# Optimization experiments

Hardware: AMD Instinct MI355X
Metric: run time of the kernel (lower is better)

## Reference

```python
import jax, jax.numpy as jnp
import numpy as np

N_NODES = 100000
N_EDGES = 500000
D = 128        # node feat dim == output dim
DT = 128       # time encoding dim
DE = 128       # edge feat dim
B = 300
K = 2
NN = 20
N_HEADS = 2
N_LAYERS = 2


def setup_inputs() -> dict:
    key = jax.random.key(0)
    ks = jax.random.split(key, 20)
    s = 0.05
    inp = {
        "node_features": jax.random.normal(ks[0], (N_NODES, D), jnp.float32) * s,
        "edge_features": jax.random.normal(ks[1], (N_EDGES, DE), jnp.float32) * s,
        "time_w": jax.random.normal(ks[2], (1, DT), jnp.float32),
        "time_b": jax.random.normal(ks[3], (DT,), jnp.float32),
        "Wq": jax.random.normal(ks[4], (N_LAYERS, D + DT, D), jnp.float32) * s,
        "Wk": jax.random.normal(ks[5], (N_LAYERS, D + DT + DE, D), jnp.float32) * s,
        "Wv": jax.random.normal(ks[6], (N_LAYERS, D + DT + DE, D), jnp.float32) * s,
        "Wo": jax.random.normal(ks[7], (N_LAYERS, D, D), jnp.float32) * s,
        "fc1": jax.random.normal(ks[8], (N_LAYERS, 2 * D, D), jnp.float32) * s,
        "fc2": jax.random.normal(ks[9], (N_LAYERS, D, D), jnp.float32) * s,
        "source_nodes": jax.random.randint(ks[10], (B,), 0, N_NODES),
        "timestamps": jax.random.uniform(ks[11], (B,), jnp.float32, 500.0, 1000.0),
        "neigh2": jax.random.randint(ks[12], (B, K, NN), 0, N_NODES),
        "eidx2": jax.random.randint(ks[13], (B, K, NN), 0, N_EDGES),
        "etimes2": jax.random.uniform(ks[14], (B, K, NN), jnp.float32, 0.0, 500.0),
        "neigh1": jax.random.randint(ks[15], (B * K * NN, K, NN), 0, N_NODES),
        "eidx1": jax.random.randint(ks[16], (B * K * NN, K, NN), 0, N_EDGES),
        "etimes1": jax.random.uniform(ks[17], (B * K * NN, K, NN), jnp.float32, 0.0, 500.0),
    }
    return inp


def reference(node_features, edge_features, time_w, time_b,
              Wq, Wk, Wv, Wo, fc1, fc2,
              source_nodes, timestamps,
              neigh2, eidx2, etimes2,
              neigh1, eidx1, etimes1):
    d = node_features.shape[1]
    dh = d // N_HEADS

    def time_enc(t):  # t: [...] -> [..., DT], TGAT-style cosine time encoding
        return jnp.cos(t[..., None] * time_w[0] + time_b)

    def hop_agg(layer, src_nodes, ts, neigh, eidx, etimes, neigh_emb):
        # neigh/eidx/etimes: [b, K, NN]; neigh_emb: [b, K, NN, d]
        b = src_nodes.shape[0]
        kn = K * NN
        src = node_features[src_nodes]                         # [b, d]
        src_t = time_enc(jnp.zeros((b,), ts.dtype))            # [b, DT]
        deltas = ts[:, None, None] - etimes                    # [b, K, NN]
        et = time_enc(deltas.reshape(b, kn))                   # [b, kn, DT]
        ef = edge_features[eidx].reshape(b, kn, -1)            # [b, kn, DE]
        ne = neigh_emb.reshape(b, kn, -1)                      # [b, kn, d]
        mask = neigh.reshape(b, kn) == 0                       # padded neighbors

        q = jnp.concatenate([src, src_t], axis=-1) @ Wq[layer]            # [b, d]
        kv_in = jnp.concatenate([ne, et, ef], axis=-1)                    # [b, kn, d+DT+DE]
        kk = kv_in @ Wk[layer]                                            # [b, kn, d]
        vv = kv_in @ Wv[layer]

        qh = q.reshape(b, N_HEADS, dh)
        kh = kk.reshape(b, kn, N_HEADS, dh)
        vh = vv.reshape(b, kn, N_HEADS, dh)
        scores = jnp.einsum('bhd,bnhd->bhn', qh, kh) / jnp.sqrt(jnp.float32(dh))
        scores = jnp.where(mask[:, None, :], jnp.float32(-1e9), scores)
        attn = jax.nn.softmax(scores, axis=-1)                            # [b, h, kn]
        out = jnp.einsum('bhn,bnhd->bhd', attn, vh).reshape(b, d) @ Wo[layer]
        merged = jnp.concatenate([out, src], axis=-1)                     # [b, 2d]
        return jax.nn.relu(merged @ fc1[layer]) @ fc2[layer]              # [b, d]

    # --- recursion unrolled (n_layers = 2) ---
    # level 0: raw node features of 2-hop neighbors
    b1 = neigh2.shape[0] * K * NN
    emb0 = node_features[neigh1.reshape(-1)].reshape(b1, K, NN, d)
    ts1 = jnp.repeat(timestamps, K * NN)
    # level 1 aggregation (attention_models[0])
    emb1 = hop_agg(0, neigh2.reshape(-1), ts1, neigh1, eidx1, etimes1, emb0)
    # level 2 aggregation (attention_models[1])
    emb2 = hop_agg(1, source_nodes, timestamps,
                   neigh2, eidx2, etimes2,
                   emb1.reshape(source_nodes.shape[0], K, NN, d))
    return emb2
```

## Files before the change

### kernel.cpp

```cpp
#include <hip/hip_runtime.h>
#include <cstdint>

typedef _Float16 half_t;
typedef _Float16 half8  __attribute__((ext_vector_type(8)));
typedef _Float16 half4_t __attribute__((ext_vector_type(4)));
typedef _Float16 h2f    __attribute__((ext_vector_type(2)));
typedef float    floatx4 __attribute__((ext_vector_type(4)));

#define KNN 40
#define KVPAD 124

#define WS_NF16    0ull
#define WS_EMB16   25600000ull
#define WS_WKVT    28672000ull
#define WS_WQ4     29065216ull
#define WS_W1A4    29196288ull
#define WS_W1B4    29327360ull
#define WS_W24     29458432ull
#define WS_QBIAS   29589504ull
#define WS_WOFTMP  29590528ull
#define WS_ZERO    29721600ull
#define WS_EF16    29721856ull
#define WS_TOTAL_FULL (WS_EF16 + 128000000ull)

__device__ __forceinline__ void ld16(const void* g, void* l) {
  __builtin_amdgcn_global_load_lds(
      (const __attribute__((address_space(1))) unsigned int*)(uintptr_t)g,
      (__attribute__((address_space(3))) unsigned int*)(uintptr_t)l, 16, 0, 0);
}

__device__ __forceinline__ float dot4(half4_t a, half4_t b, float s) {
  s = __builtin_amdgcn_fdot2((h2f){a[0], a[1]}, (h2f){b[0], b[1]}, s, false);
  s = __builtin_amdgcn_fdot2((h2f){a[2], a[3]}, (h2f){b[2], b[3]}, s, false);
  return s;
}

__global__ __launch_bounds__(256) void cvt_kernel(
    const float* __restrict__ src, half_t* __restrict__ dst, int n8) {
  int stride = gridDim.x * 256;
  for (int i = blockIdx.x * 256 + threadIdx.x; i < n8; i += stride) {
    float4 a = *((const float4*)src + 2 * (size_t)i);
    float4 b = *((const float4*)src + 2 * (size_t)i + 1);
    half8 h;
    h[0] = (half_t)a.x; h[1] = (half_t)a.y; h[2] = (half_t)a.z; h[3] = (half_t)a.w;
    h[4] = (half_t)b.x; h[5] = (half_t)b.y; h[6] = (half_t)b.z; h[7] = (half_t)b.w;
    *((half8*)dst + i) = h;
  }
}

#define PK_DECODE(t) int l = (t) >> 14; int u = (t) & 16383; \
  int d4 = u >> 9; int v = u & 511; int j = v >> 2; int e = v & 3;

__global__ __launch_bounds__(256) void precompute_w(
    const float* __restrict__ Wq, const float* __restrict__ Wk,
    const float* __restrict__ Wv, const float* __restrict__ Wo,
    const float* __restrict__ fc1, const float* __restrict__ fc2,
    const float* __restrict__ time_b,
    half_t* __restrict__ WkvT, float* __restrict__ qbias,
    float* __restrict__ woftmp, half_t* __restrict__ Wq4,
    half_t* __restrict__ W1b4, half_t* __restrict__ W24,
    half_t* __restrict__ zrow)
{
  int blk = blockIdx.x, tid = threadIdx.x;
  if (blk < 768) {
    int t = blk * 256 + tid;
    int l = t / 98304;
    int r = t - l * 98304;
    int n = r / 384;
    int k = r - n * 384;
    float vv = (n < 128) ? Wk[l * 49152 + k * 128 + n]
                         : Wv[l * 49152 + k * 128 + (n - 128)];
    WkvT[t] = (half_t)vv;
  } else if (blk == 768) {
    if (tid < 128) zrow[tid] = (half_t)0.f;
    int l = tid >> 7, j = tid & 127;
    float s = 0.f;
    for (int d = 0; d < 128; ++d)
      s += cosf(time_b[d]) * Wq[l * 32768 + (128 + d) * 128 + j];
    qbias[l * 128 + j] = s;
  } else if (blk < 897) {
    int t = (blk - 769) * 256 + tid;
    int l = t >> 14;
    int r = t & 16383;
    int dd = r >> 7, j = r & 127;
    float s = 0.f;
    for (int m = 0; m < 128; ++m)
      s += Wo[l * 16384 + dd * 128 + m] * fc1[l * 32768 + m * 128 + j];
    woftmp[t] = s;
  } else if (blk < 1025) {
    int t = (blk - 897) * 256 + tid;
    PK_DECODE(t);
    Wq4[t] = (half_t)Wq[l * 32768 + (4 * d4 + e) * 128 + j];
  } else if (blk < 1153) {
    int t = (blk - 1025) * 256 + tid;
    PK_DECODE(t);
    W1b4[t] = (half_t)fc1[l * 32768 + (128 + 4 * d4 + e) * 128 + j];
  } else {
    int t = (blk - 1153) * 256 + tid;
    PK_DECODE(t);
    W24[t] = (half_t)fc2[l * 16384 + (4 * d4 + e) * 128 + j];
  }
}

__global__ __launch_bounds__(256) void precompute_w2(
    const float* __restrict__ woftmp, half_t* __restrict__ W1a4) {
  int t = blockIdx.x * 256 + threadIdx.x;
  PK_DECODE(t);
  W1a4[t] = (half_t)woftmp[l * 16384 + (4 * d4 + e) * 128 + j];
}

template <bool EF16, bool L1DIR>
__global__ __launch_bounds__(512, 4) void hop_kernel(
    const float*  __restrict__ nf,
    const half_t* __restrict__ ne16,
    const half_t* __restrict__ ef16,
    const float*  __restrict__ ef32,
    const int*    __restrict__ src_idx,
    const float*  __restrict__ tsv,
    const int*    __restrict__ neigh,
    const int*    __restrict__ eidx,
    const float*  __restrict__ etimes,
    const float*  __restrict__ tw,
    const float*  __restrict__ tb,
    const half_t* __restrict__ Wq4_l,
    const float*  __restrict__ qbias_l,
    const half_t* __restrict__ WkvT_l,
    const half_t* __restrict__ W1a4_l,
    const half_t* __restrict__ W1b4_l,
    const half_t* __restrict__ W24_l,
    const half_t* __restrict__ zrow,
    half_t* __restrict__ out16,
    float*  __restrict__ out32)
{
  __shared__ __align__(16) char smem[71360];
  half_t* BTs  = (half_t*)(smem + 32768);
  half_t* kvT  = (half_t*)(smem + 32768);
  float*  tw_s = (float*)(smem + 65536);
  float*  tb_s = (float*)(smem + 66048);
  float*  qs   = (float*)(smem + 66560);
  half_t* s16  = (half_t*)(smem + 68096);
  half_t* aO16 = (half_t*)(smem + 68864);
  half_t* h116 = (half_t*)(smem + 69632);
  float*  scs  = (float*)(smem + 70400);

  const int tid = threadIdx.x;
  const int bbase = blockIdx.x * 3;
  const int lane = tid & 63, wv = tid >> 6;
  const int l15 = lane & 15, q4 = lane >> 4;
  const int wm = (wv & 1) * 64, wn = (wv >> 1) * 64;

  if (tid < 128) { tw_s[tid] = tw[tid]; tb_s[tid] = tb[tid]; }
  if (tid < 96) {
    int g = tid >> 5, d4 = tid & 31;
    float4 v4 = *(const float4*)(nf + (size_t)src_idx[bbase + g] * 128 + d4 * 4);
    half4_t h;
    h[0] = (half_t)v4.x; h[1] = (half_t)v4.y; h[2] = (half_t)v4.z; h[3] = (half_t)v4.w;
    *(half4_t*)(s16 + g * 128 + d4 * 4) = h;
  }

  const int r = wv * 16 + l15;
  const bool valid = (r < 120);
  float dval = 0.f;
  const half_t* pNE = zrow + q4 * 8;
  const half_t* pEF = zrow + q4 * 8;
  if (valid) {
    int g = r / 40, n = r - g * 40;
    int bg = bbase + g;
    int rowidx = bg * KNN + n;
    dval = tsv[L1DIR ? bg : (bg / 40)] - etimes[rowidx];
    pNE = (L1DIR ? ne16 + (size_t)rowidx * 128
                 : ne16 + (size_t)neigh[rowidx] * 128) + q4 * 8;
    if (EF16) pEF = ef16 + (size_t)eidx[rowidx] * 128 + q4 * 8;
  }
  const float* gbe32 = nullptr;
  const int rr = tid >> 2, pp = tid & 3;
  if (!EF16 && rr < 120) {
    int g2 = rr / 40, n2 = rr - g2 * 40;
    gbe32 = ef32 + (size_t)eidx[(bbase + g2) * KNN + n2] * 128 + pp * 16;
  }

  const half_t* bBase = WkvT_l + (size_t)(2 * wv * 16 + l15) * 384 + q4 * 8;

  floatx4 acc[4][4];
  #pragma unroll
  for (int mi = 0; mi < 4; ++mi)
    #pragma unroll
    for (int ni = 0; ni < 4; ++ni) acc[mi][ni] = (floatx4){0.f, 0.f, 0.f, 0.f};

  auto issueA = [&](const half_t* p, int koff, char* buf) {
    ld16(p + koff,      buf + wv * 2048);
    ld16(p + koff + 32, buf + wv * 2048 + 1024);
  };
  auto issueB = [&](int kc) {
    const half_t* bp = bBase + kc * 64;
    ld16(bp,          (char*)BTs + wv * 4096);
    ld16(bp + 32,     (char*)BTs + wv * 4096 + 1024);
    ld16(bp + 6144,   (char*)BTs + wv * 4096 + 2048);
    ld16(bp + 6176,   (char*)BTs + wv * 4096 + 3072);
  };
  auto cosA = [&](int koff, char* buf) {
    #pragma unroll
    for (int i = 0; i < 2; ++i) {
      int c = i * 4 + q4;
      half8 h;
      #pragma unroll
      for (int j = 0; j < 8; ++j) {
        float ang = __builtin_fmaf(dval, tw_s[koff + c * 8 + j], tb_s[koff + c * 8 + j]);
        h[j] = valid ? (half_t)__cosf(ang) : (half_t)0.f;
      }
      *(half8*)(buf + wv * 2048 + i * 1024 + lane * 16) = h;
    }
  };
  auto efA32 = [&](int koff, char* buf) {
    half8 h0 = {}, h1 = {};
    if (rr < 120) {
      const float* gb = gbe32 + koff;
      float4 v0 = ((const float4*)gb)[0];
      float4 v1 = ((const float4*)gb)[1];
      float4 v2 = ((const float4*)gb)[2];
      float4 v3 = ((const float4*)gb)[3];
      h0[0] = (half_t)v0.x; h0[1] = (half_t)v0.y; h0[2] = (half_t)v0.z; h0[3] = (half_t)v0.w;
      h0[4] = (half_t)v1.x; h0[5] = (half_t)v1.y; h0[6] = (half_t)v1.z; h0[7] = (half_t)v1.w;
      h1[0] = (half_t)v2.x; h1[1] = (half_t)v2.y; h1[2] = (half_t)v2.z; h1[3] = (half_t)v2.w;
      h1[4] = (half_t)v3.x; h1[5] = (half_t)v3.y; h1[6] = (half_t)v3.z; h1[7] = (half_t)v3.w;
    }
    half_t* Ad = (half_t*)buf + (((rr >> 4) * 8) + 2 * pp) * 128 + (rr & 15) * 8;
    *(half8*)Ad = h0;
    *(half8*)(Ad + 128) = h1;
  };
  auto mfma_step = [&](const char* abuf) {
    #pragma unroll
    for (int ks = 0; ks < 2; ++ks) {
      int c = ks * 4 + q4;
      half8 a[4];
      #pragma unroll
      for (int mi = 0; mi < 4; ++mi)
        a[mi] = *(const half8*)((const half_t*)abuf + (((wm >> 4) + mi) * 8 + c) * 128 + l15 * 8);
      #pragma unroll
      for (int ni = 0; ni < 4; ++ni) {
        half8 bfr = *(const half8*)(BTs + (((wn >> 4) + ni) * 8 + c) * 128 + l15 * 8);
        #pragma unroll
        for (int mi = 0; mi < 4; ++mi)
          acc[mi][ni] = __builtin_amdgcn_mfma_f32_16x16x32_f16(a[mi], bfr, acc[mi][ni], 0, 0, 0);
      }
    }
  };

  issueA(pNE, 0, smem);
  issueA(pNE, 64, smem + 16384);
  {
    const char* sw = (const char*)Wq4_l + wv * 4096 + lane * 16;
    char* dw = (char*)BTs + wv * 4096;
    ld16(sw, dw); ld16(sw + 1024, dw + 1024);
    ld16(sw + 2048, dw + 2048); ld16(sw + 3072, dw + 3072);
  }
  __syncthreads();

  if (tid < 384) {
    int gq = tid >> 7, jj = tid & 127;
    float s = qbias_l[jj];
    #pragma unroll 8
    for (int d4 = 0; d4 < 32; ++d4) {
      half4_t w = *(const half4_t*)(BTs + (d4 * 128 + jj) * 4);
      half4_t a = *(const half4_t*)(s16 + gq * 128 + d4 * 4);
      s = dot4(w, a, s);
    }
    qs[gq * 128 + jj] = s;
  }
  __syncthreads();

  issueB(0); __syncthreads(); mfma_step(smem);          __syncthreads();
  cosA(0, smem);
  issueB(1); __syncthreads(); mfma_step(smem + 16384);  __syncthreads();
  cosA(64, smem + 16384);
  issueB(2); __syncthreads(); mfma_step(smem);          __syncthreads();
  if (EF16) issueA(pEF, 0, smem); else efA32(0, smem);
  issueB(3); __syncthreads(); mfma_step(smem + 16384);  __syncthreads();
  if (EF16) issueA(pEF, 64, smem + 16384); else efA32(64, smem + 16384);
  issueB(4); __syncthreads(); mfma_step(smem);          __syncthreads();
  issueB(5); __syncthreads(); mfma_step(smem + 16384);  __syncthreads();

  {
    const char* sw = (const char*)W1a4_l + wv * 4096 + lane * 16;
    char* dw = smem + wv * 4096;
    ld16(sw, dw); ld16(sw + 1024, dw + 1024);
    ld16(sw + 2048, dw + 2048); ld16(sw + 3072, dw + 3072);
  }

  if (wv < 4) {
    #pragma unroll
    for (int mi = 0; mi < 4; ++mi) {
      int row0 = wm + mi * 16 + q4 * 4;
      if (row0 < 120) {
        #pragma unroll
        for (int ni = 0; ni < 4; ++ni) {
          int col = wn + ni * 16 + l15;
          half4_t h;
          h[0] = (half_t)acc[mi][ni][0]; h[1] = (half_t)acc[mi][ni][1];
          h[2] = (half_t)acc[mi][ni][2]; h[3] = (half_t)acc[mi][ni][3];
          *(half4_t*)(kvT + col * KVPAD + row0) = h;
        }
      }
    }
  }
  __syncthreads();

  if (tid < 240) {
    int g = tid / 80;
    int rem = tid - g * 80;
    int h = rem / 40;
    int n = rem - h * 40;
    bool masked = (neigh[(bbase + g) * KNN + n] == 0);
    const float* qrow = qs + g * 128 + h * 64;
    int row = g * 40 + n;
    float s = 0.f;
    #pragma unroll 8
    for (int d = 0; d < 64; ++d)
      s += qrow[d] * (float)kvT[(h * 64 + d) * KVPAD + row];
    scs[tid] = masked ? -1e9f : s * 0.125f;
  }
  __syncthreads();

  if (wv < 6) {
    float v = (lane < 40) ? scs[wv * 40 + lane] : -1e30f;
    float m = v;
    #pragma unroll
    for (int o = 32; o; o >>= 1) m = fmaxf(m, __shfl_xor(m, o));
    float e = (lane < 40) ? __expf(v - m) : 0.f;
    float ssum = e;
    #pragma unroll
    for (int o = 32; o; o >>= 1) ssum += __shfl_xor(ssum, o);
    if (lane < 40) scs[wv * 40 + lane] = e / ssum;
  }
  if (wv >= 4) {
    #pragma unroll
    for (int mi = 0; mi < 4; ++mi) {
      int row0 = wm + mi * 16 + q4 * 4;
      if (row0 < 120) {
        #pragma unroll
        for (int ni = 0; ni < 4; ++ni) {
          int col = wn - 128 + ni * 16 + l15;
          half4_t h;
          h[0] = (half_t)acc[mi][ni][0]; h[1] = (half_t)acc[mi][ni][1];
          h[2] = (half_t)acc[mi][ni][2]; h[3] = (half_t)acc[mi][ni][3];
          *(half4_t*)(kvT + col * KVPAD + row0) = h;
        }
      }
    }
  }
  __syncthreads();

  if (tid < 384) {
    int g = tid >> 7, dcol = tid & 127, h = dcol >> 6;
    const float* attn = scs + (g * 2 + h) * 40;
    const half_t* vcol = kvT + dcol * KVPAD + g * 40;
    float s = 0.f;
    #pragma unroll 8
    for (int n = 0; n < 40; ++n) s += attn[n] * (float)vcol[n];
    aO16[g * 128 + dcol] = (half_t)s;
  }
  __syncthreads();

  {
    const char* sw = (const char*)W1b4_l + wv * 4096 + lane * 16;
    char* dw = (char*)BTs + wv * 4096;
    ld16(sw, dw); ld16(sw + 1024, dw + 1024);
    ld16(sw + 2048, dw + 2048); ld16(sw + 3072, dw + 3072);
  }
  float p1 = 0.f;
  if (tid < 384) {
    int g = tid >> 7, jj = tid & 127;
    #pragma unroll 8
    for (int d4 = 0; d4 < 32; ++d4) {
      half4_t w = *(const half4_t*)((const half_t*)smem + (d4 * 128 + jj) * 4);
      half4_t a = *(const half4_t*)(aO16 + g * 128 + d4 * 4);
      p1 = dot4(w, a, p1);
    }
  }
  __syncthreads();

  {
    const char* sw = (const char*)W24_l + wv * 4096 + lane * 16;
    char* dw = smem + wv * 4096;
    ld16(sw, dw); ld16(sw + 1024, dw + 1024);
    ld16(sw + 2048, dw + 2048); ld16(sw + 3072, dw + 3072);
  }
  if (tid < 384) {
    int g = tid >> 7, jj = tid & 127;
    float p2 = p1;
    #pragma unroll 8
    for (int d4 = 0; d4 < 32; ++d4) {
      half4_t w = *(const half4_t*)(BTs + (d4 * 128 + jj) * 4);
      half4_t a = *(const half4_t*)(s16 + g * 128 + d4 * 4);
      p2 = dot4(w, a, p2);
    }
    h116[g * 128 + jj] = (half_t)fmaxf(p2, 0.f);
  }
  __syncthreads();

  if (tid < 384) {
    int g = tid >> 7, ii = tid & 127;
    float s = 0.f;
    #pragma unroll 8
    for (int j4 = 0; j4 < 32; ++j4) {
      half4_t w = *(const half4_t*)((const half_t*)smem + (j4 * 128 + ii) * 4);
      half4_t a = *(const half4_t*)(h116 + g * 128 + j4 * 4);
      s = dot4(w, a, s);
    }
    if (L1DIR) out32[(size_t)(bbase + g) * 128 + ii] = s;
    else       out16[(size_t)(bbase + g) * 128 + ii] = (half_t)s;
  }
}

extern "C" void kernel_launch(void* const* d_in, const int* in_sizes, int n_in,
                              void* d_out, int out_size, void* d_ws, size_t ws_size,
                              hipStream_t stream) {
  const float* nf      = (const float*)d_in[0];
  const float* ef      = (const float*)d_in[1];
  const float* tw      = (const float*)d_in[2];
  const float* tb      = (const float*)d_in[3];
  const float* Wq      = (const float*)d_in[4];
  const float* Wk      = (const float*)d_in[5];
  const float* Wv      = (const float*)d_in[6];
  const float* Wo      = (const float*)d_in[7];
  const float* fc1     = (const float*)d_in[8];
  const float* fc2     = (const float*)d_in[9];
  const int*   srcn    = (const int*)d_in[10];
  const float* ts      = (const float*)d_in[11];
  const int*   neigh2  = (const int*)d_in[12];
  const int*   eidx2   = (const int*)d_in[13];
  const float* etimes2 = (const float*)d_in[14];
  const int*   neigh1  = (const int*)d_in[15];
  const int*   eidx1   = (const int*)d_in[16];
  const float* etimes1 = (const float*)d_in[17];

  char* ws = (char*)d_ws;
  half_t* nf16   = (half_t*)(ws + WS_NF16);
  half_t* emb116 = (half_t*)(ws + WS_EMB16);
  half_t* WkvT16 = (half_t*)(ws + WS_WKVT);
  half_t* Wq4    = (half_t*)(ws + WS_WQ4);
  half_t* W1a4   = (half_t*)(ws + WS_W1A4);
  half_t* W1b4   = (half_t*)(ws + WS_W1B4);
  half_t* W24    = (half_t*)(ws + WS_W24);
  float*  qbias  = (float*)(ws + WS_QBIAS);
  float*  woftmp = (float*)(ws + WS_WOFTMP);
  half_t* zrow   = (half_t*)(ws + WS_ZERO);
  half_t* ef16   = (half_t*)(ws + WS_EF16);

  bool full = (ws_size >= WS_TOTAL_FULL);

  cvt_kernel<<<dim3(2048), dim3(256), 0, stream>>>(nf, nf16, 1600000);
  if (full)
    cvt_kernel<<<dim3(4096), dim3(256), 0, stream>>>(ef, ef16, 8000000);
  precompute_w<<<dim3(1281), dim3(256), 0, stream>>>(
      Wq, Wk, Wv, Wo, fc1, fc2, tb, WkvT16, qbias, woftmp, Wq4, W1b4, W24, zrow);
  precompute_w2<<<dim3(128), dim3(256), 0, stream>>>(woftmp, W1a4);

  if (full) {
    hop_kernel<true, false><<<dim3(4000), dim3(512), 0, stream>>>(
        nf, nf16, ef16, ef, neigh2, ts, neigh1, eidx1, etimes1, tw, tb,
        Wq4, qbias, WkvT16, W1a4, W1b4, W24, zrow, emb116, nullptr);
    hop_kernel<true, true><<<dim3(100), dim3(512), 0, stream>>>(
        nf, emb116, ef16, ef, srcn, ts, neigh2, eidx2, etimes2, tw, tb,
        Wq4 + 16384, qbias + 128, WkvT16 + 98304, W1a4 + 16384, W1b4 + 16384,
        W24 + 16384, zrow, emb116, (float*)d_out);
  } else {
    hop_kernel<false, false><<<dim3(4000), dim3(512), 0, stream>>>(
        nf, nf16, ef16, ef, neigh2, ts, neigh1, eidx1, etimes1, tw, tb,
        Wq4, qbias, WkvT16, W1a4, W1b4, W24, zrow, emb116, nullptr);
    hop_kernel<false, true><<<dim3(100), dim3(512), 0, stream>>>(
        nf, emb116, ef16, ef, srcn, ts, neigh2, eidx2, etimes2, tw, tb,
        Wq4 + 16384, qbias + 128, WkvT16 + 98304, W1a4 + 16384, W1b4 + 16384,
        W24 + 16384, zrow, emb116, (float*)d_out);
  }
}
```

Before: 737.0 us.

## Restructure hop kernel to load A tiles once and read weights directly from global

```diff
diff --git a/kernel.cpp b/kernel.cpp
--- a/kernel.cpp
+++ b/kernel.cpp
@@ -18,10 +18,7 @@
 #define WS_W1B4    29327360ull
 #define WS_W24     29458432ull
 #define WS_QBIAS   29589504ull
-#define WS_WOFTMP  29590528ull
-#define WS_ZERO    29721600ull
 #define WS_EF16    29721856ull
-#define WS_TOTAL_FULL (WS_EF16 + 128000000ull)
 
 __device__ __forceinline__ void ld16(const void* g, void* l) {
   __builtin_amdgcn_global_load_lds(
@@ -57,9 +54,8 @@
     const float* __restrict__ fc1, const float* __restrict__ fc2,
     const float* __restrict__ time_b,
     half_t* __restrict__ WkvT, float* __restrict__ qbias,
-    float* __restrict__ woftmp, half_t* __restrict__ Wq4,
-    half_t* __restrict__ W1b4, half_t* __restrict__ W24,
-    half_t* __restrict__ zrow)
+    half_t* __restrict__ Wq4, half_t* __restrict__ W1a4,
+    half_t* __restrict__ W1b4, half_t* __restrict__ W24)
 {
   int blk = blockIdx.x, tid = threadIdx.x;
   if (blk < 768) {
@@ -72,7 +68,6 @@
                          : Wv[l * 49152 + k * 128 + (n - 128)];
     WkvT[t] = (half_t)vv;
   } else if (blk == 768) {
-    if (tid < 128) zrow[tid] = (half_t)0.f;
     int l = tid >> 7, j = tid & 127;
     float s = 0.f;
     for (int d = 0; d < 128; ++d)
@@ -80,13 +75,11 @@
     qbias[l * 128 + j] = s;
   } else if (blk < 897) {
     int t = (blk - 769) * 256 + tid;
-    int l = t >> 14;
-    int r = t & 16383;
-    int dd = r >> 7, j = r & 127;
+    PK_DECODE(t);
     float s = 0.f;
     for (int m = 0; m < 128; ++m)
-      s += Wo[l * 16384 + dd * 128 + m] * fc1[l * 32768 + m * 128 + j];
-    woftmp[t] = s;
+      s += Wo[l * 16384 + (4 * d4 + e) * 128 + m] * fc1[l * 32768 + m * 128 + j];
+    W1a4[t] = (half_t)s;
   } else if (blk < 1025) {
     int t = (blk - 897) * 256 + tid;
     PK_DECODE(t);
@@ -102,19 +95,11 @@
   }
 }
 
-__global__ __launch_bounds__(256) void precompute_w2(
-    const float* __restrict__ woftmp, half_t* __restrict__ W1a4) {
-  int t = blockIdx.x * 256 + threadIdx.x;
-  PK_DECODE(t);
-  W1a4[t] = (half_t)woftmp[l * 16384 + (4 * d4 + e) * 128 + j];
-}
-
-template <bool EF16, bool L1DIR>
+template <bool L1DIR>
 __global__ __launch_bounds__(512, 4) void hop_kernel(
-    const float*  __restrict__ nf,
+    const half_t* __restrict__ nf16,
     const half_t* __restrict__ ne16,
     const half_t* __restrict__ ef16,
-    const float*  __restrict__ ef32,
     const int*    __restrict__ src_idx,
     const float*  __restrict__ tsv,
     const int*    __restrict__ neigh,
@@ -128,20 +113,19 @@
     const half_t* __restrict__ W1a4_l,
     const half_t* __restrict__ W1b4_l,
     const half_t* __restrict__ W24_l,
-    const half_t* __restrict__ zrow,
     half_t* __restrict__ out16,
     float*  __restrict__ out32)
 {
-  __shared__ __align__(16) char smem[71360];
-  half_t* BTs  = (half_t*)(smem + 32768);
-  half_t* kvT  = (half_t*)(smem + 32768);
+  __shared__ __align__(16) char smem[71104];
+  half_t* A    = (half_t*)smem;
+  half_t* kvT  = (half_t*)smem;
   float*  tw_s = (float*)(smem + 65536);
   float*  tb_s = (float*)(smem + 66048);
-  float*  qs   = (float*)(smem + 66560);
-  half_t* s16  = (half_t*)(smem + 68096);
-  half_t* aO16 = (half_t*)(smem + 68864);
-  half_t* h116 = (half_t*)(smem + 69632);
-  float*  scs  = (float*)(smem + 70400);
+  float*  dvals= (float*)(smem + 66560);
+  float*  qs   = (float*)(smem + 67072);
+  float*  scs  = (float*)(smem + 68608);
+  half_t* aO16 = (half_t*)(smem + 69568);
+  half_t* h116 = (half_t*)(smem + 70336);
 
   const int tid = threadIdx.x;
   const int bbase = blockIdx.x * 3;
@@ -150,36 +134,49 @@
   const int wm = (wv & 1) * 64, wn = (wv >> 1) * 64;
 
   if (tid < 128) { tw_s[tid] = tw[tid]; tb_s[tid] = tb[tid]; }
-  if (tid < 96) {
-    int g = tid >> 5, d4 = tid & 31;
-    float4 v4 = *(const float4*)(nf + (size_t)src_idx[bbase + g] * 128 + d4 * 4);
-    half4_t h;
-    h[0] = (half_t)v4.x; h[1] = (half_t)v4.y; h[2] = (half_t)v4.z; h[3] = (half_t)v4.w;
-    *(half4_t*)(s16 + g * 128 + d4 * 4) = h;
-  }
 
   const int r = wv * 16 + l15;
   const bool valid = (r < 120);
   float dval = 0.f;
-  const half_t* pNE = zrow + q4 * 8;
-  const half_t* pEF = zrow + q4 * 8;
+  const half_t* pNE = nf16;
+  const half_t* pEF = nf16;
   if (valid) {
     int g = r / 40, n = r - g * 40;
     int bg = bbase + g;
     int rowidx = bg * KNN + n;
     dval = tsv[L1DIR ? bg : (bg / 40)] - etimes[rowidx];
-    pNE = (L1DIR ? ne16 + (size_t)rowidx * 128
-                 : ne16 + (size_t)neigh[rowidx] * 128) + q4 * 8;
-    if (EF16) pEF = ef16 + (size_t)eidx[rowidx] * 128 + q4 * 8;
-  }
-  const float* gbe32 = nullptr;
-  const int rr = tid >> 2, pp = tid & 3;
-  if (!EF16 && rr < 120) {
-    int g2 = rr / 40, n2 = rr - g2 * 40;
-    gbe32 = ef32 + (size_t)eidx[(bbase + g2) * KNN + n2] * 128 + pp * 16;
-  }
-
-  const half_t* bBase = WkvT_l + (size_t)(2 * wv * 16 + l15) * 384 + q4 * 8;
+    pNE = L1DIR ? ne16 + (size_t)rowidx * 128
+                : ne16 + (size_t)neigh[rowidx] * 128;
+    pEF = ef16 + (size_t)eidx[rowidx] * 128;
+  }
+  if (q4 == 0) dvals[r] = dval;
+  pNE += q4 * 8; pEF += q4 * 8;
+
+  {
+    char* d0 = smem + wv * 2048;
+    ld16(pNE,      d0);
+    ld16(pNE + 32, d0 + 1024);
+    ld16(pNE + 64, d0 + 16384);
+    ld16(pNE + 96, d0 + 16384 + 1024);
+    ld16(pEF,      d0 + 32768);
+    ld16(pEF + 32, d0 + 32768 + 1024);
+    ld16(pEF + 64, d0 + 49152);
+    ld16(pEF + 96, d0 + 49152 + 1024);
+  }
+
+  if (tid < 384) {
+    int gq = tid >> 7, jq = tid & 127;
+    const half_t* srow = nf16 + (size_t)src_idx[bbase + gq] * 128;
+    float s = qbias_l[jq];
+    #pragma unroll 8
+    for (int d4 = 0; d4 < 32; ++d4) {
+      half4_t w = *(const half4_t*)(Wq4_l + (d4 * 128 + jq) * 4);
+      half4_t a = *(const half4_t*)(srow + d4 * 4);
+      s = dot4(w, a, s);
+    }
+    qs[gq * 128 + jq] = s;
+  }
+  __syncthreads();
 
   floatx4 acc[4][4];
   #pragma unroll
@@ -187,105 +184,39 @@
     #pragma unroll
     for (int ni = 0; ni < 4; ++ni) acc[mi][ni] = (floatx4){0.f, 0.f, 0.f, 0.f};
 
-  auto issueA = [&](const half_t* p, int koff, char* buf) {
-    ld16(p + koff,      buf + wv * 2048);
-    ld16(p + koff + 32, buf + wv * 2048 + 1024);
-  };
-  auto issueB = [&](int kc) {
-    const half_t* bp = bBase + kc * 64;
-    ld16(bp,          (char*)BTs + wv * 4096);
-    ld16(bp + 32,     (char*)BTs + wv * 4096 + 1024);
-    ld16(bp + 6144,   (char*)BTs + wv * 4096 + 2048);
-    ld16(bp + 6176,   (char*)BTs + wv * 4096 + 3072);
-  };
-  auto cosA = [&](int koff, char* buf) {
-    #pragma unroll
-    for (int i = 0; i < 2; ++i) {
-      int c = i * 4 + q4;
-      half8 h;
-      #pragma unroll
-      for (int j = 0; j < 8; ++j) {
-        float ang = __builtin_fmaf(dval, tw_s[koff + c * 8 + j], tb_s[koff + c * 8 + j]);
-        h[j] = valid ? (half_t)__cosf(ang) : (half_t)0.f;
+  const int mt0 = wm >> 4;
+  #pragma unroll
+  for (int kc = 0; kc < 6; ++kc) {
+    const int grp = (kc < 2) ? kc : kc - 2;
+    #pragma unroll
+    for (int ks = 0; ks < 2; ++ks) {
+      const int c = ks * 4 + q4;
+      half8 a[4];
+      if (kc == 2 || kc == 3) {
+        const int colbase = (kc - 2) * 64 + ks * 32 + q4 * 8;
+        #pragma unroll
+        for (int mi = 0; mi < 4; ++mi) {
+          float dv = dvals[wm + mi * 16 + l15];
+          #pragma unroll
+          for (int j = 0; j < 8; ++j)
+            a[mi][j] = (half_t)__cosf(__builtin_fmaf(dv, tw_s[colbase + j], tb_s[colbase + j]));
+        }
+      } else {
+        #pragma unroll
+        for (int mi = 0; mi < 4; ++mi)
+          a[mi] = *(const half8*)(A + grp * 8192 + (((mt0 + mi) * 8 + c) * 16 + l15) * 8);
       }
-      *(half8*)(buf + wv * 2048 + i * 1024 + lane * 16) = h;
-    }
-  };
-  auto efA32 = [&](int koff, char* buf) {
-    half8 h0 = {}, h1 = {};
-    if (rr < 120) {
-      const float* gb = gbe32 + koff;
-      float4 v0 = ((const float4*)gb)[0];
-      float4 v1 = ((const float4*)gb)[1];
-      float4 v2 = ((const float4*)gb)[2];
-      float4 v3 = ((const float4*)gb)[3];
-      h0[0] = (half_t)v0.x; h0[1] = (half_t)v0.y; h0[2] = (half_t)v0.z; h0[3] = (half_t)v0.w;
-      h0[4] = (half_t)v1.x; h0[5] = (half_t)v1.y; h0[6] = (half_t)v1.z; h0[7] = (half_t)v1.w;
-      h1[0] = (half_t)v2.x; h1[1] = (half_t)v2.y; h1[2] = (half_t)v2.z; h1[3] = (half_t)v2.w;
-      h1[4] = (half_t)v3.x; h1[5] = (half_t)v3.y; h1[6] = (half_t)v3.z; h1[7] = (half_t)v3.w;
-    }
-    half_t* Ad = (half_t*)buf + (((rr >> 4) * 8) + 2 * pp) * 128 + (rr & 15) * 8;
-    *(half8*)Ad = h0;
-    *(half8*)(Ad + 128) = h1;
-  };
-  auto mfma_step = [&](const char* abuf) {
-    #pragma unroll
-    for (int ks = 0; ks < 2; ++ks) {
-      int c = ks * 4 + q4;
-      half8 a[4];
-      #pragma unroll
-      for (int mi = 0; mi < 4; ++mi)
-        a[mi] = *(const half8*)((const half_t*)abuf + (((wm >> 4) + mi) * 8 + c) * 128 + l15 * 8);
+      const int koff = kc * 64 + ks * 32 + q4 * 8;
       #pragma unroll
       for (int ni = 0; ni < 4; ++ni) {
-        half8 bfr = *(const half8*)(BTs + (((wn >> 4) + ni) * 8 + c) * 128 + l15 * 8);
+        half8 b = *(const half8*)(WkvT_l + (size_t)(wn + ni * 16 + l15) * 384 + koff);
         #pragma unroll
         for (int mi = 0; mi < 4; ++mi)
-          acc[mi][ni] = __builtin_amdgcn_mfma_f32_16x16x32_f16(a[mi], bfr, acc[mi][ni], 0, 0, 0);
+          acc[mi][ni] = __builtin_amdgcn_mfma_f32_16x16x32_f16(a[mi], b, acc[mi][ni], 0, 0, 0);
       }
     }
-  };
-
-  issueA(pNE, 0, smem);
-  issueA(pNE, 64, smem + 16384);
-  {
-    const char* sw = (const char*)Wq4_l + wv * 4096 + lane * 16;
-    char* dw = (char*)BTs + wv * 4096;
-    ld16(sw, dw); ld16(sw + 1024, dw + 1024);
-    ld16(sw + 2048, dw + 2048); ld16(sw + 3072, dw + 3072);
-  }
-  __syncthreads();
-
-  if (tid < 384) {
-    int gq = tid >> 7, jj = tid & 127;
-    float s = qbias_l[jj];
-    #pragma unroll 8
-    for (int d4 = 0; d4 < 32; ++d4) {
-      half4_t w = *(const half4_t*)(BTs + (d4 * 128 + jj) * 4);
-      half4_t a = *(const half4_t*)(s16 + gq * 128 + d4 * 4);
-      s = dot4(w, a, s);
-    }
-    qs[gq * 128 + jj] = s;
-  }
-  __syncthreads();
-
-  issueB(0); __syncthreads(); mfma_step(smem);          __syncthreads();
-  cosA(0, smem);
-  issueB(1); __syncthreads(); mfma_step(smem + 16384);  __syncthreads();
-  cosA(64, smem + 16384);
-  issueB(2); __syncthreads(); mfma_step(smem);          __syncthreads();
-  if (EF16) issueA(pEF, 0, smem); else efA32(0, smem);
-  issueB(3); __syncthreads(); mfma_step(smem + 16384);  __syncthreads();
-  if (EF16) issueA(pEF, 64, smem + 16384); else efA32(64, smem + 16384);
-  issueB(4); __syncthreads(); mfma_step(smem);          __syncthreads();
-  issueB(5); __syncthreads(); mfma_step(smem + 16384);  __syncthreads();
-
-  {
-    const char* sw = (const char*)W1a4_l + wv * 4096 + lane * 16;
-    char* dw = smem + wv * 4096;
-    ld16(sw, dw); ld16(sw + 1024, dw + 1024);
-    ld16(sw + 2048, dw + 2048); ld16(sw + 3072, dw + 3072);
-  }
+  }
+  __syncthreads();
 
   if (wv < 4) {
     #pragma unroll
@@ -361,40 +292,20 @@
   }
   __syncthreads();
 
-  {
-    const char* sw = (const char*)W1b4_l + wv * 4096 + lane * 16;
-    char* dw = (char*)BTs + wv * 4096;
-    ld16(sw, dw); ld16(sw + 1024, dw + 1024);
-    ld16(sw + 2048, dw + 2048); ld16(sw + 3072, dw + 3072);
-  }
-  float p1 = 0.f;
   if (tid < 384) {
     int g = tid >> 7, jj = tid & 127;
+    const half_t* srow = nf16 + (size_t)src_idx[bbase + g] * 128;
+    float s = 0.f;
     #pragma unroll 8
     for (int d4 = 0; d4 < 32; ++d4) {
-      half4_t w = *(const half4_t*)((const half_t*)smem + (d4 * 128 + jj) * 4);
-      half4_t a = *(const half4_t*)(aO16 + g * 128 + d4 * 4);
-      p1 = dot4(w, a, p1);
-    }
-  }
-  __syncthreads();
-
-  {
-    const char* sw = (const char*)W24_l + wv * 4096 + lane * 16;
-    char* dw = smem + wv * 4096;
-    ld16(sw, dw); ld16(sw + 1024, dw + 1024);
-    ld16(sw + 2048, dw + 2048); ld16(sw + 3072, dw + 3072);
-  }
-  if (tid < 384) {
-    int g = tid >> 7, jj = tid & 127;
-    float p2 = p1;
-    #pragma unroll 8
-    for (int d4 = 0; d4 < 32; ++d4) {
-      half4_t w = *(const half4_t*)(BTs + (d4 * 128 + jj) * 4);
-      half4_t a = *(const half4_t*)(s16 + g * 128 + d4 * 4);
-      p2 = dot4(w, a, p2);
-    }
-    h116[g * 128 + jj] = (half_t)fmaxf(p2, 0.f);
+      half4_t wa = *(const half4_t*)(W1a4_l + (d4 * 128 + jj) * 4);
+      half4_t aa = *(const half4_t*)(aO16 + g * 128 + d4 * 4);
+      s = dot4(wa, aa, s);
+      half4_t wb = *(const half4_t*)(W1b4_l + (d4 * 128 + jj) * 4);
+      half4_t ab = *(const half4_t*)(srow + d4 * 4);
+      s = dot4(wb, ab, s);
+    }
+    h116[g * 128 + jj] = (half_t)fmaxf(s, 0.f);
   }
   __syncthreads();
 
@@ -403,7 +314,7 @@
     float s = 0.f;
     #pragma unroll 8
     for (int j4 = 0; j4 < 32; ++j4) {
-      half4_t w = *(const half4_t*)((const half_t*)smem + (j4 * 128 + ii) * 4);
+      half4_t w = *(const half4_t*)(W24_l + (j4 * 128 + ii) * 4);
       half4_t a = *(const half4_t*)(h116 + g * 128 + j4 * 4);
       s = dot4(w, a, s);
     }
@@ -443,34 +354,20 @@
   half_t* W1b4   = (half_t*)(ws + WS_W1B4);
   half_t* W24    = (half_t*)(ws + WS_W24);
   float*  qbias  = (float*)(ws + WS_QBIAS);
-  float*  woftmp = (float*)(ws + WS_WOFTMP);
-  half_t* zrow   = (half_t*)(ws + WS_ZERO);
   half_t* ef16   = (half_t*)(ws + WS_EF16);
-
-  bool full = (ws_size >= WS_TOTAL_FULL);
+  (void)ws_size;
 
   cvt_kernel<<<dim3(2048), dim3(256), 0, stream>>>(nf, nf16, 1600000);
-  if (full)
-    cvt_kernel<<<dim3(4096), dim3(256), 0, stream>>>(ef, ef16, 8000000);
+  cvt_kernel<<<dim3(4096), dim3(256), 0, stream>>>(ef, ef16, 8000000);
   precompute_w<<<dim3(1281), dim3(256), 0, stream>>>(
-      Wq, Wk, Wv, Wo, fc1, fc2, tb, WkvT16, qbias, woftmp, Wq4, W1b4, W24, zrow);
-  precompute_w2<<<dim3(128), dim3(256), 0, stream>>>(woftmp, W1a4);
-
-  if (full) {
-    hop_kernel<true, false><<<dim3(4000), dim3(512), 0, stream>>>(
-        nf, nf16, ef16, ef, neigh2, ts, neigh1, eidx1, etimes1, tw, tb,
-        Wq4, qbias, WkvT16, W1a4, W1b4, W24, zrow, emb116, nullptr);
-    hop_kernel<true, true><<<dim3(100), dim3(512), 0, stream>>>(
-        nf, emb116, ef16, ef, srcn, ts, neigh2, eidx2, etimes2, tw, tb,
-        Wq4 + 16384, qbias + 128, WkvT16 + 98304, W1a4 + 16384, W1b4 + 16384,
-        W24 + 16384, zrow, emb116, (float*)d_out);
-  } else {
-    hop_kernel<false, false><<<dim3(4000), dim3(512), 0, stream>>>(
-        nf, nf16, ef16, ef, neigh2, ts, neigh1, eidx1, etimes1, tw, tb,
-        Wq4, qbias, WkvT16, W1a4, W1b4, W24, zrow, emb116, nullptr);
-    hop_kernel<false, true><<<dim3(100), dim3(512), 0, stream>>>(
-        nf, emb116, ef16, ef, srcn, ts, neigh2, eidx2, etimes2, tw, tb,
-        Wq4 + 16384, qbias + 128, WkvT16 + 98304, W1a4 + 16384, W1b4 + 16384,
-        W24 + 16384, zrow, emb116, (float*)d_out);
-  }
-}
+      Wq, Wk, Wv, Wo, fc1, fc2, tb, WkvT16, qbias, Wq4, W1a4, W1b4, W24);
+
+  hop_kernel<false><<<dim3(4000), dim3(512), 0, stream>>>(
+      nf16, nf16, ef16, neigh2, ts, neigh1, eidx1, etimes1, tw, tb,
+      Wq4, qbias, WkvT16, W1a4, W1b4, W24, emb116, nullptr);
+
+  hop_kernel<true><<<dim3(100), dim3(512), 0, stream>>>(
+      nf16, emb116, ef16, srcn, ts, neigh2, eidx2, etimes2, tw, tb,
+      Wq4 + 16384, qbias + 128, WkvT16 + 98304, W1a4 + 16384, W1b4 + 16384,
+      W24 + 16384, emb116, (float*)d_out);
+}
```

After: 846.2 us. +14.8%, slower.
